# Performance work log

Hardware: AMD Instinct MI355X
Metric: run time of the kernel (lower is better)

Reference implementation:

```python
import jax, jax.numpy as jnp
import numpy as np

N_NODES = 100000
N_EDGES = 1600000
D = 128
NEG_SLOPE = 0.01  # torch F.leaky_relu default


def setup_inputs() -> dict:
    key = jax.random.key(0)
    k1, k2, k3, k4, k5, k6 = jax.random.split(key, 6)
    input = jax.random.normal(k1, (N_NODES, D), dtype=jnp.float32)
    edge_row = jax.random.randint(k2, (N_EDGES,), 0, N_NODES, dtype=jnp.int32)
    edge_col = jax.random.randint(k3, (N_EDGES,), 0, N_NODES, dtype=jnp.int32)
    edge_val = jax.random.uniform(k4, (N_EDGES,), dtype=jnp.float32)
    # learned params: W1: Linear(D, D, bias=False), W2: Linear(2D, D, bias=False)
    # torch stores weight as [out, in]; apply as x @ W.T
    bound1 = 1.0 / np.sqrt(D)
    bound2 = 1.0 / np.sqrt(2 * D)
    W1 = jax.random.uniform(k5, (D, D), dtype=jnp.float32, minval=-bound1, maxval=bound1)
    W2 = jax.random.uniform(k6, (D, 2 * D), dtype=jnp.float32, minval=-bound2, maxval=bound2)
    return {"input": input, "edge_row": edge_row, "edge_col": edge_col,
            "edge_val": edge_val, "W1": W1, "W2": W2}


def reference(input, edge_row, edge_col, edge_val, W1, W2):
    # proj_input = W1(input)
    proj = input @ W1.T                                   # [N, D]
    # neighboor = spmm(adj, proj): out[i] = sum_e val[e] * proj[col[e]] for row[e]==i
    msg = edge_val[:, None] * proj[edge_col]              # [E, D]
    neigh = jax.ops.segment_sum(msg, edge_row, num_segments=input.shape[0])  # [N, D]
    h = jnp.concatenate([input + neigh, input * neigh], axis=-1)  # [N, 2D]
    return jax.nn.leaky_relu(h @ W2.T, NEG_SLOPE)         # [N, D]
```

## Files before the change

kernel.cpp:

```cpp
#include <hip/hip_runtime.h>

#define DIM 128
#define BROWS 128
#define BCAP 3072
#define BK_EDGES 2048

typedef __attribute__((ext_vector_type(8))) short short8;
typedef __attribute__((ext_vector_type(4))) float f32x4;

__device__ __forceinline__ unsigned short f2bf(float f) {
    unsigned u = __float_as_uint(f);
    u += 0x7fffu + ((u >> 16) & 1u);
    return (unsigned short)(u >> 16);
}
__device__ __forceinline__ float bf2f(unsigned short b) {
    return __uint_as_float(((unsigned)b) << 16);
}

__global__ void k_pre(const float4* __restrict__ in, const float* __restrict__ W1,
                      const float* __restrict__ W2, unsigned short* __restrict__ inputb,
                      unsigned short* __restrict__ w1b, unsigned short* __restrict__ w2b,
                      int* __restrict__ gcur, int n4, int nCvt, int nbuk) {
    int b = blockIdx.x;
    if (b < nCvt) {
        int i = b * 256 + threadIdx.x;
        if (i < n4) {
            float4 v = in[i];
            *(ushort4*)(inputb + (long)i * 4) =
                make_ushort4(f2bf(v.x), f2bf(v.y), f2bf(v.z), f2bf(v.w));
        }
    } else if (b < nCvt + 192) {
        int idx = (b - nCvt) * 256 + threadIdx.x;
        if (idx < 16384)      w1b[idx] = f2bf(W1[idx]);
        else                  w2b[idx - 16384] = f2bf(W2[idx - 16384]);
    } else {
        int i = (b - nCvt - 192) * 256 + threadIdx.x;
        if (i < nbuk) gcur[i] = 0;
    }
}

__global__ __launch_bounds__(256) void k_bucket(const int* __restrict__ er,
                                                const int* __restrict__ ec,
                                                const float* __restrict__ ev,
                                                int* __restrict__ gcur,
                                                int2* __restrict__ edata, int E, int nbuk) {
    __shared__ int lhist[800];
    __shared__ int lpos[800];
    for (int b = threadIdx.x; b < nbuk; b += 256) lhist[b] = 0;
    __syncthreads();
    int e0 = blockIdx.x * BK_EDGES;
    for (int j = 0; j < BK_EDGES; j += 256) {
        int e = e0 + j + threadIdx.x;
        if (e < E) atomicAdd(&lhist[er[e] >> 7], 1);
    }
    __syncthreads();
    for (int b = threadIdx.x; b < nbuk; b += 256) {
        int c = lhist[b];
        int g = (c > 0) ? atomicAdd(&gcur[b], c) : 0;
        lpos[b] = b * BCAP + g;
    }
    __syncthreads();
    for (int j = 0; j < BK_EDGES; j += 256) {
        int e = e0 + j + threadIdx.x;
        if (e < E) {
            int r = er[e], b = r >> 7;
            int p = atomicAdd(&lpos[b], 1);
            if (p < (b + 1) * BCAP)
                edata[p] = make_int2(((r & 127) << 17) | ec[e], __float_as_int(ev[e]));
        }
    }
}

__global__ __launch_bounds__(256) void k_csr(int2* __restrict__ edata,
                                             const int* __restrict__ gcur,
                                             int* __restrict__ rs, int* __restrict__ re) {
    __shared__ int2 sed[BCAP];
    __shared__ int hist[BROWS];
    __shared__ int scan[BROWS];
    __shared__ int lcur[BROWS];
    int b = blockIdx.x, tid = threadIdx.x;
    int cnt = gcur[b]; if (cnt > BCAP) cnt = BCAP;
    int2* ed = edata + (long)b * BCAP;
    if (tid < BROWS) hist[tid] = 0;
    for (int i = tid; i < cnt; i += 256) sed[i] = ed[i];
    __syncthreads();
    for (int i = tid; i < cnt; i += 256) atomicAdd(&hist[sed[i].x >> 17], 1);
    __syncthreads();
    if (tid < BROWS) scan[tid] = hist[tid];
    __syncthreads();
    for (int off = 1; off < BROWS; off <<= 1) {
        int v = (tid < BROWS && tid >= off) ? scan[tid - off] : 0;
        __syncthreads();
        if (tid < BROWS) scan[tid] += v;
        __syncthreads();
    }
    if (tid < BROWS) {
        int excl = scan[tid] - hist[tid];
        lcur[tid] = excl;
        int row = b * BROWS + tid;
        rs[row] = b * BCAP + excl;
        re[row] = b * BCAP + excl + hist[tid];
    }
    __syncthreads();
    for (int i = tid; i < cnt; i += 256) {
        int2 v = sed[i];
        int p = atomicAdd(&lcur[v.x >> 17], 1);
        ed[p] = make_int2(v.x & 0x1FFFF, v.y);
    }
}

__global__ __launch_bounds__(256) void k_gather(const unsigned short* __restrict__ xb,
                                                const int2* __restrict__ edata,
                                                const int* __restrict__ rs,
                                                const int* __restrict__ re,
                                                unsigned short* __restrict__ aggb, int N) {
    int wave = threadIdx.x >> 6, lane = threadIdx.x & 63;
    int row = blockIdx.x * 4 + wave;
    if (row >= N) return;
    int beg = rs[row], end = re[row];
    int g = lane >> 3, s = lane & 7;
    float pa[8], pb[8];
#pragma unroll
    for (int k = 0; k < 8; ++k) { pa[k] = 0.f; pb[k] = 0.f; }
    const int4* x4 = (const int4*)xb;
    for (int p = beg; p < end; p += 8) {
        int idx = p + g;
        int2 e = (idx < end) ? edata[idx] : make_int2(0, 0);
        float v = __int_as_float(e.y);
        long base = (long)e.x * 16;
        int4 ua = x4[base + s];
        int4 ub = x4[base + 8 + s];
        const unsigned* wa = (const unsigned*)&ua;
        const unsigned* wb = (const unsigned*)&ub;
#pragma unroll
        for (int k = 0; k < 4; ++k) {
            pa[2 * k]     += v * __uint_as_float(wa[k] << 16);
            pa[2 * k + 1] += v * __uint_as_float(wa[k] & 0xffff0000u);
            pb[2 * k]     += v * __uint_as_float(wb[k] << 16);
            pb[2 * k + 1] += v * __uint_as_float(wb[k] & 0xffff0000u);
        }
    }
#pragma unroll
    for (int m = 8; m <= 32; m <<= 1) {
#pragma unroll
        for (int k = 0; k < 8; ++k) {
            pa[k] += __shfl_xor(pa[k], m);
            pb[k] += __shfl_xor(pb[k], m);
        }
    }
    if (g == 0) {
        short8 oa, ob;
#pragma unroll
        for (int k = 0; k < 8; ++k) {
            oa[k] = (short)f2bf(pa[k]);
            ob[k] = (short)f2bf(pb[k]);
        }
        *(short8*)(aggb + (long)row * DIM + s * 8)      = oa;
        *(short8*)(aggb + (long)row * DIM + 64 + s * 8) = ob;
    }
}

__global__ __launch_bounds__(256, 4) void k_fused(const unsigned short* __restrict__ aggb,
                                                  const unsigned short* __restrict__ inputb,
                                                  const unsigned short* __restrict__ w1b,
                                                  const unsigned short* __restrict__ w2b,
                                                  float* __restrict__ out, int N) {
    __shared__ __align__(16) unsigned short sh[2 * 64 * 136];
    int w = threadIdx.x >> 6, lane = threadIdx.x & 63;
    int quad = lane >> 4, lq = lane & 15;
    int blk0 = blockIdx.x * 64;
    unsigned short* sh0 = sh;
    unsigned short* sh1 = sh + 64 * 136;

    short8 b1[2][4];
#pragma unroll
    for (int ntl = 0; ntl < 2; ++ntl)
#pragma unroll
        for (int kb = 0; kb < 4; ++kb)
            b1[ntl][kb] = *(const short8*)(w1b + ((w * 2 + ntl) * 16 + lq) * DIM +
                                           kb * 32 + quad * 8);

#pragma unroll
    for (int mt = 0; mt < 4; ++mt) {
        short8 afr[4];
        {
            int row = blk0 + mt * 16 + lq; if (row >= N) row = N - 1;
#pragma unroll
            for (int kb = 0; kb < 4; ++kb)
                afr[kb] = *(const short8*)(aggb + (long)row * DIM + kb * 32 + quad * 8);
        }
#pragma unroll
        for (int ntl = 0; ntl < 2; ++ntl) {
            f32x4 c = {0.f, 0.f, 0.f, 0.f};
#pragma unroll
            for (int kb = 0; kb < 4; ++kb)
                c = __builtin_amdgcn_mfma_f32_16x16x32_bf16(afr[kb], b1[ntl][kb], c, 0, 0, 0);
            int nt = w * 2 + ntl;
#pragma unroll
            for (int rg = 0; rg < 4; ++rg) {
                int r = blk0 + mt * 16 + quad * 4 + rg;
                int rr = (r < N) ? r : (N - 1);
                float x = bf2f(inputb[(long)rr * DIM + nt * 16 + lq]);
                float nb = c[rg];
                int off = (mt * 16 + quad * 4 + rg) * 136 + nt * 16 + lq;
                sh0[off] = f2bf(x + nb);
                sh1[off] = f2bf(x * nb);
            }
        }
    }

    short8 b2[2][8];
#pragma unroll
    for (int ntl = 0; ntl < 2; ++ntl)
#pragma unroll
        for (int kb = 0; kb < 8; ++kb)
            b2[ntl][kb] = *(const short8*)(w2b + ((w * 2 + ntl) * 16 + lq) * 256 +
                                           kb * 32 + quad * 8);
    __syncthreads();

#pragma unroll
    for (int mt = 0; mt < 4; ++mt) {
        int arow = (mt * 16 + lq) * 136;
        short8 a0[4], a1[4];
#pragma unroll
        for (int kb = 0; kb < 4; ++kb) {
            a0[kb] = *(const short8*)(sh0 + arow + kb * 32 + quad * 8);
            a1[kb] = *(const short8*)(sh1 + arow + kb * 32 + quad * 8);
        }
#pragma unroll
        for (int ntl = 0; ntl < 2; ++ntl) {
            f32x4 c = {0.f, 0.f, 0.f, 0.f};
#pragma unroll
            for (int kb = 0; kb < 4; ++kb)
                c = __builtin_amdgcn_mfma_f32_16x16x32_bf16(a0[kb], b2[ntl][kb], c, 0, 0, 0);
#pragma unroll
            for (int kb = 0; kb < 4; ++kb)
                c = __builtin_amdgcn_mfma_f32_16x16x32_bf16(a1[kb], b2[ntl][kb + 4], c, 0, 0, 0);
            int nt = w * 2 + ntl;
#pragma unroll
            for (int rg = 0; rg < 4; ++rg) {
                int r = blk0 + mt * 16 + quad * 4 + rg;
                if (r < N) {
                    float v = c[rg];
                    v = (v > 0.f) ? v : 0.01f * v;
                    out[(long)r * DIM + nt * 16 + lq] = v;
                }
            }
        }
    }
}

extern "C" void kernel_launch(void* const* d_in, const int* in_sizes, int n_in,
                              void* d_out, int out_size, void* d_ws, size_t ws_size,
                              hipStream_t stream) {
    const float* input = (const float*)d_in[0];
    const int*   er    = (const int*)d_in[1];
    const int*   ec    = (const int*)d_in[2];
    const float* ev    = (const float*)d_in[3];
    const float* W1    = (const float*)d_in[4];
    const float* W2    = (const float*)d_in[5];
    int N = in_sizes[0] / DIM;
    int E = in_sizes[1];
    float* out = (float*)d_out;
    int nbuk = (N + BROWS - 1) / BROWS;

    int* ws = (int*)d_ws;
    int* gcur = ws;
    int2* edata = (int2*)(ws + 1024);
    int* rs = (int*)(edata + (long)nbuk * BCAP);
    int* re = rs + (long)nbuk * BROWS;
    unsigned short* w1b = (unsigned short*)(re + (long)nbuk * BROWS);
    unsigned short* w2b = w1b + 16384;
    unsigned short* inputb = w2b + 32768;
    unsigned short* aggb = inputb + (long)N * DIM;

    int n4 = N * (DIM / 4);
    int nCvt = (n4 + 255) / 256;
    int nZero = (nbuk + 255) / 256;
    k_pre<<<nCvt + 192 + nZero, 256, 0, stream>>>(
        (const float4*)input, W1, W2, inputb, w1b, w2b, gcur, n4, nCvt, nbuk);

    k_bucket<<<(E + BK_EDGES - 1) / BK_EDGES, 256, 0, stream>>>(
        er, ec, ev, gcur, edata, E, nbuk);

    k_csr<<<nbuk, 256, 0, stream>>>(edata, gcur, rs, re);

    k_gather<<<(N + 3) / 4, 256, 0, stream>>>(inputb, edata, rs, re, aggb, N);

    k_fused<<<(N + 63) / 64, 256, 0, stream>>>(aggb, inputb, w1b, w2b, out, N);
}
```

Before: 280.3 us.

## Assign one 16-lane group per row in gather with shuffled edge broadcast

The gather kernel changes from one wave per row (8 edge groups of 8 lanes, then a cross-group shuffle reduction) to four rows per wave, each handled by 16 lanes. Each lane owns 8 feature elements, and edge indices and values are loaded cooperatively and broadcast with shuffles, four edges at a time. This removes the final reduction shuffles and keeps more wave lanes busy on low-degree rows, which should raise memory-level parallelism. In exchange, each wave's loop trip count follows the largest degree among its four rows, so padded iterations gather row 0 with zero weight.

Result: no change. 275.9 us (-1.6%).

```diff
diff --git a/kernel.cpp b/kernel.cpp
--- a/kernel.cpp
+++ b/kernel.cpp
@@ -114,49 +114,65 @@
                                                 const int* __restrict__ rs,
                                                 const int* __restrict__ re,
                                                 unsigned short* __restrict__ aggb, int N) {
-    int wave = threadIdx.x >> 6, lane = threadIdx.x & 63;
-    int row = blockIdx.x * 4 + wave;
-    if (row >= N) return;
-    int beg = rs[row], end = re[row];
-    int g = lane >> 3, s = lane & 7;
-    float pa[8], pb[8];
-#pragma unroll
-    for (int k = 0; k < 8; ++k) { pa[k] = 0.f; pb[k] = 0.f; }
+    int tid = threadIdx.x, lane = tid & 63, wave = tid >> 6;
+    int grp = lane >> 4, s = lane & 15;
+    int row = blockIdx.x * 16 + wave * 4 + grp;
+    int beg = 0, end = 0;
+    if (row < N) { beg = rs[row]; end = re[row]; }
+    int deg = end - beg;
+    int m = deg;
+    m = max(m, __shfl_xor(m, 16));
+    m = max(m, __shfl_xor(m, 32));
+    float pa[8];
+#pragma unroll
+    for (int k = 0; k < 8; ++k) pa[k] = 0.f;
     const int4* x4 = (const int4*)xb;
-    for (int p = beg; p < end; p += 8) {
-        int idx = p + g;
-        int2 e = (idx < end) ? edata[idx] : make_int2(0, 0);
-        float v = __int_as_float(e.y);
-        long base = (long)e.x * 16;
-        int4 ua = x4[base + s];
-        int4 ub = x4[base + 8 + s];
-        const unsigned* wa = (const unsigned*)&ua;
-        const unsigned* wb = (const unsigned*)&ub;
-#pragma unroll
-        for (int k = 0; k < 4; ++k) {
-            pa[2 * k]     += v * __uint_as_float(wa[k] << 16);
-            pa[2 * k + 1] += v * __uint_as_float(wa[k] & 0xffff0000u);
-            pb[2 * k]     += v * __uint_as_float(wb[k] << 16);
-            pb[2 * k + 1] += v * __uint_as_float(wb[k] & 0xffff0000u);
-        }
-    }
-#pragma unroll
-    for (int m = 8; m <= 32; m <<= 1) {
-#pragma unroll
-        for (int k = 0; k < 8; ++k) {
-            pa[k] += __shfl_xor(pa[k], m);
-            pb[k] += __shfl_xor(pb[k], m);
-        }
-    }
-    if (g == 0) {
-        short8 oa, ob;
-#pragma unroll
-        for (int k = 0; k < 8; ++k) {
-            oa[k] = (short)f2bf(pa[k]);
-            ob[k] = (short)f2bf(pb[k]);
-        }
-        *(short8*)(aggb + (long)row * DIM + s * 8)      = oa;
-        *(short8*)(aggb + (long)row * DIM + 64 + s * 8) = ob;
+    int bsrc = lane & 48;
+
+#define ACC8(U, V)                                                         \
+    {                                                                      \
+        const unsigned* wp_ = (const unsigned*)&(U);                       \
+        pa[0] += (V) * __uint_as_float(wp_[0] << 16);                      \
+        pa[1] += (V) * __uint_as_float(wp_[0] & 0xffff0000u);              \
+        pa[2] += (V) * __uint_as_float(wp_[1] << 16);                      \
+        pa[3] += (V) * __uint_as_float(wp_[1] & 0xffff0000u);              \
+        pa[4] += (V) * __uint_as_float(wp_[2] << 16);                      \
+        pa[5] += (V) * __uint_as_float(wp_[2] & 0xffff0000u);              \
+        pa[6] += (V) * __uint_as_float(wp_[3] << 16);                      \
+        pa[7] += (V) * __uint_as_float(wp_[3] & 0xffff0000u);              \
+    }
+
+    for (int c0 = 0; c0 < m; c0 += 16) {
+        int idx = beg + c0 + s;
+        int2 ed = (idx < end) ? edata[idx] : make_int2(0, 0);
+        int nc = m - c0; if (nc > 16) nc = 16;
+        nc = (nc + 3) & ~3;
+        for (int j = 0; j < nc; j += 4) {
+            int cx0 = __shfl(ed.x, bsrc + j);
+            int cx1 = __shfl(ed.x, bsrc + j + 1);
+            int cx2 = __shfl(ed.x, bsrc + j + 2);
+            int cx3 = __shfl(ed.x, bsrc + j + 3);
+            float v0 = __int_as_float(__shfl(ed.y, bsrc + j));
+            float v1 = __int_as_float(__shfl(ed.y, bsrc + j + 1));
+            float v2 = __int_as_float(__shfl(ed.y, bsrc + j + 2));
+            float v3 = __int_as_float(__shfl(ed.y, bsrc + j + 3));
+            int4 u0 = x4[(long)cx0 * 16 + s];
+            int4 u1 = x4[(long)cx1 * 16 + s];
+            int4 u2 = x4[(long)cx2 * 16 + s];
+            int4 u3 = x4[(long)cx3 * 16 + s];
+            ACC8(u0, v0);
+            ACC8(u1, v1);
+            ACC8(u2, v2);
+            ACC8(u3, v3);
+        }
+    }
+#undef ACC8
+
+    if (row < N) {
+        short8 o;
+#pragma unroll
+        for (int k = 0; k < 8; ++k) o[k] = (short)f2bf(pa[k]);
+        *(short8*)(aggb + (long)row * DIM + s * 8) = o;
     }
 }
 
@@ -285,7 +301,7 @@
 
     k_csr<<<nbuk, 256, 0, stream>>>(edata, gcur, rs, re);
 
-    k_gather<<<(N + 3) / 4, 256, 0, stream>>>(inputb, edata, rs, re, aggb, N);
+    k_gather<<<(N + 15) / 16, 256, 0, stream>>>(inputb, edata, rs, re, aggb, N);
 
     k_fused<<<(N + 63) / 64, 256, 0, stream>>>(aggb, inputb, w1b, w2b, out, N);
 }
```
